# Kernel optimization log

Hardware: AMD Instinct MI355X
Metric: run time of the kernel (lower is better)

The kernel has to match this reference:

```python
import jax, jax.numpy as jnp
import numpy as np

ALPHA = 0.2      # LeakyReLU negative slope
BN_EPS = 1e-5    # torch BatchNorm1d default eps

N_NODES = 50000
N_EDGES = 1600000
DIM_IN = 128
DIM_HID = 64
DIM_OUT = 128
NUM_HEADS = 8


def gat_layer(feat, src, dst, W, a, gamma, beta):
    """One GATLayer forward (dropout disabled, BatchNorm in training mode
    i.e. normalized with batch statistics over the node dimension)."""
    n = feat.shape[0]
    dh = W.shape[1]
    msg = feat @ W                                  # [N, dh]
    attn_src = msg @ a[:dh]                         # [N]
    attn_dst = msg @ a[dh:]                         # [N]
    scores = jax.nn.leaky_relu(attn_src[src] + attn_dst[dst], ALPHA)  # [E]
    scores = scores - scores.max()                  # global max-subtract (as in source)
    e = jnp.exp(scores)                             # [E]
    denom = jax.ops.segment_sum(e, dst, num_segments=n) + 1e-10       # [N]
    coef = e / denom[dst]                           # [E] segment-softmax
    out = jax.ops.segment_sum(msg[src] * coef[:, None], dst, num_segments=n)  # [N, dh]
    # BatchNorm1d (training-mode batch stats, biased variance)
    mean = out.mean(axis=0)
    var = out.var(axis=0)
    out = (out - mean) * jax.lax.rsqrt(var + BN_EPS) * gamma + beta
    return out


def setup_inputs() -> dict:
    key = jax.random.key(0)
    ks = jax.random.split(key, 10)
    feat = jax.random.normal(ks[0], (N_NODES, DIM_IN), dtype=jnp.float32)
    edges = jax.random.randint(ks[1], (2, N_EDGES), 0, N_NODES)

    def xavier(k, shape):
        fan_in, fan_out = shape[0], shape[-1]
        lim = np.sqrt(6.0 / (fan_in + fan_out)).astype(np.float32)
        return jax.random.uniform(k, shape, jnp.float32, -lim, lim)

    W_heads = xavier(ks[2], (NUM_HEADS, DIM_IN, DIM_HID))
    a_heads = xavier(ks[3], (NUM_HEADS, 2 * DIM_HID))
    gamma_h = jnp.ones((NUM_HEADS, DIM_HID), jnp.float32)
    beta_h = jnp.zeros((NUM_HEADS, DIM_HID), jnp.float32)
    W_out = xavier(ks[4], (NUM_HEADS * DIM_HID, DIM_OUT))
    a_out = xavier(ks[5], (2 * DIM_OUT,))
    gamma_o = jnp.ones((DIM_OUT,), jnp.float32)
    beta_o = jnp.zeros((DIM_OUT,), jnp.float32)
    W_res = xavier(ks[6], (DIM_IN, DIM_OUT))
    b_res = jnp.zeros((DIM_OUT,), jnp.float32)
    return {"feat": feat, "edges": edges, "W_heads": W_heads, "a_heads": a_heads,
            "gamma_h": gamma_h, "beta_h": beta_h, "W_out": W_out, "a_out": a_out,
            "gamma_o": gamma_o, "beta_o": beta_o, "W_res": W_res, "b_res": b_res}


def reference(feat, edges, W_heads, a_heads, gamma_h, beta_h,
              W_out, a_out, gamma_o, beta_o, W_res, b_res):
    src, dst = edges[0], edges[1]
    # python loop over a small fixed number of heads keeps peak memory low
    head_outs = [gat_layer(feat, src, dst, W_heads[h], a_heads[h], gamma_h[h], beta_h[h])
                 for h in range(NUM_HEADS)]
    x = jnp.concatenate(head_outs, axis=-1)          # [N, H*dh]
    x = gat_layer(x, src, dst, W_out, a_out, gamma_o, beta_o)  # [N, dout]
    x = x + feat @ W_res + b_res                     # residual Linear
    return x
```

## Files before the change

### kernel.cpp

```cpp
#include <hip/hip_runtime.h>
#include <math.h>

#define N_NODES 50000
#define N_EDGES 1600000
#define DIM_IN  128
#define DIM_HID 64
#define NHEADS  8
#define HDIM    (NHEADS*DIM_HID)
#define DIM_OUT 128
#define SMBLK   1024
#define MAXBLK  512
#define LDK     72
#define INV_N   2e-5f
#define CSBLK   400

typedef __attribute__((ext_vector_type(2))) unsigned short us2;
typedef __attribute__((ext_vector_type(4))) unsigned short us4;
typedef __attribute__((ext_vector_type(8))) unsigned short us8;
typedef __attribute__((ext_vector_type(8))) short bf16x8;
typedef __attribute__((ext_vector_type(4))) float f32x4;

__device__ __forceinline__ float leaky(float x) { return x >= 0.f ? x : 0.2f * x; }
__device__ __forceinline__ float bf2f(unsigned short h) {
  return __uint_as_float(((unsigned)h) << 16);
}
__device__ __forceinline__ unsigned short f2bf(float f) {
  unsigned u = __float_as_uint(f);
  unsigned r = (u + 0x7fffu + ((u >> 16) & 1u)) >> 16;
  return (unsigned short)r;
}
__device__ __forceinline__ float bn_scale(float sum, float sq, float g) {
  float mean = sum * INV_N;
  float var = sq * INV_N - mean * mean;
  return g * rsqrtf(var + 1e-5f);
}

__global__ void prep_kernel(const float* __restrict__ feat, const float* __restrict__ Wh,
                            const float* __restrict__ Wres,
                            unsigned short* __restrict__ feat_bf,
                            unsigned short* __restrict__ Bt1,
                            unsigned short* __restrict__ Btr) {
  int b = blockIdx.x;
  if (b < 6250) {
    int i = b * 256 + threadIdx.x;
    float4 v = *reinterpret_cast<const float4*>(&feat[(size_t)i * 4]);
    us4 o;
    o[0] = f2bf(v.x); o[1] = f2bf(v.y); o[2] = f2bf(v.z); o[3] = f2bf(v.w);
    *reinterpret_cast<us4*>(&feat_bf[(size_t)i * 4]) = o;
  } else if (b < 6506) {
    int idx = (b - 6250) * 256 + threadIdx.x;
    int n = idx >> 7, k = idx & 127;
    Bt1[idx] = f2bf(Wh[(n >> 6) * (DIM_IN * DIM_HID) + k * DIM_HID + (n & 63)]);
  } else {
    int idx = (b - 6506) * 256 + threadIdx.x;
    int n = idx >> 7, k = idx & 127;
    Btr[idx] = f2bf(Wres[k * DIM_OUT + n]);
  }
}

__global__ void foldw2_kernel(const float* __restrict__ W,
                              const float* __restrict__ colsum, const float* __restrict__ colsq,
                              const float* __restrict__ gamma,
                              unsigned short* __restrict__ Bt) {
  int idx = blockIdx.x * 256 + threadIdx.x;
  if (idx >= DIM_OUT * HDIM) return;
  int n = idx >> 9, k = idx & 511;
  float sc = bn_scale(colsum[k], colsq[k], gamma[k]);
  Bt[idx] = f2bf(W[k * DIM_OUT + n] * sc);
}

__global__ void bias2_kernel(const float* __restrict__ W,
                             const float* __restrict__ colsum, const float* __restrict__ colsq,
                             const float* __restrict__ gamma, const float* __restrict__ beta,
                             float* __restrict__ bias2) {
  int j = threadIdx.x;
  if (j >= DIM_OUT) return;
  float s = 0.f;
  for (int c = 0; c < HDIM; ++c) {
    float mean = colsum[c] * INV_N;
    float sc = bn_scale(colsum[c], colsq[c], gamma[c]);
    float shift = beta[c] - mean * sc;
    s = fmaf(shift, W[c * DIM_OUT + j], s);
  }
  bias2[j] = s;
}

template<int OUTBF>
__global__ __launch_bounds__(256) void gemm_mfma(
    const unsigned short* __restrict__ A, const unsigned short* __restrict__ Bt,
    void* __restrict__ Cout, const float* __restrict__ bias,
    int M, int N, int K) {
  __shared__ unsigned short As[128 * LDK];
  __shared__ unsigned short Bs[128 * LDK];
  const int tid = threadIdx.x;
  const int lane = tid & 63, wid = tid >> 6;
  const int wr = wid >> 1, wc = wid & 1;
  const int l15 = lane & 15, lhi = lane >> 4;
  const int m0 = blockIdx.y * 128, n0 = blockIdx.x * 128;
  const int srow = tid >> 3;
  const int sc8 = (tid - srow) & 7;
  f32x4 acc[4][4];
#pragma unroll
  for (int i = 0; i < 4; ++i)
#pragma unroll
    for (int j = 0; j < 4; ++j) acc[i][j] = f32x4{0.f, 0.f, 0.f, 0.f};

  for (int k0 = 0; k0 < K; k0 += 64) {
    __syncthreads();
#pragma unroll
    for (int p = 0; p < 4; ++p) {
      int row = p * 32 + srow;
      us8 va = {0, 0, 0, 0, 0, 0, 0, 0};
      int gr = m0 + row;
      if (gr < M) va = *reinterpret_cast<const us8*>(&A[(size_t)gr * K + k0 + sc8 * 8]);
      *reinterpret_cast<us8*>(&As[row * LDK + sc8 * 8]) = va;
      us8 vb = {0, 0, 0, 0, 0, 0, 0, 0};
      int gn = n0 + row;
      if (gn < N) vb = *reinterpret_cast<const us8*>(&Bt[(size_t)gn * K + k0 + sc8 * 8]);
      *reinterpret_cast<us8*>(&Bs[row * LDK + sc8 * 8]) = vb;
    }
    __syncthreads();
#pragma unroll
    for (int kk = 0; kk < 2; ++kk) {
      bf16x8 af[4], bfr[4];
#pragma unroll
      for (int i = 0; i < 4; ++i)
        af[i] = *reinterpret_cast<const bf16x8*>(&As[(wr * 64 + i * 16 + l15) * LDK + kk * 32 + lhi * 8]);
#pragma unroll
      for (int j = 0; j < 4; ++j)
        bfr[j] = *reinterpret_cast<const bf16x8*>(&Bs[(wc * 64 + j * 16 + l15) * LDK + kk * 32 + lhi * 8]);
#pragma unroll
      for (int i = 0; i < 4; ++i)
#pragma unroll
        for (int j = 0; j < 4; ++j)
          acc[i][j] = __builtin_amdgcn_mfma_f32_16x16x32_bf16(af[i], bfr[j], acc[i][j], 0, 0, 0);
    }
  }
#pragma unroll
  for (int j = 0; j < 4; ++j) {
    int col = n0 + wc * 64 + j * 16 + l15;
    float bb = bias ? bias[col] : 0.f;
#pragma unroll
    for (int i = 0; i < 4; ++i) {
      f32x4 v = acc[i][j];
#pragma unroll
      for (int t = 0; t < 4; ++t) {
        int row = m0 + wr * 64 + i * 16 + lhi * 4 + t;
        if (row < M) {
          float o = v[t] + bb;
          if (OUTBF) ((unsigned short*)Cout)[(size_t)row * N + col] = f2bf(o);
          else       ((float*)Cout)[(size_t)row * N + col] = o;
        }
      }
    }
  }
}

__global__ __launch_bounds__(256) void attn1_kernel(
    const unsigned short* __restrict__ msg, const float* __restrict__ a_heads,
    float* __restrict__ asrc, float* __restrict__ adst, int Nn) {
  int lane = threadIdx.x & 63;
  int n = blockIdx.x * 4 + (threadIdx.x >> 6);
  if (n >= Nn) return;
  us8 v = *reinterpret_cast<const us8*>(&msg[(size_t)n * HDIM + lane * 8]);
  int h = lane >> 3, p0 = (lane & 7) * 8;
  float s = 0.f, d = 0.f;
#pragma unroll
  for (int j = 0; j < 8; ++j) {
    float f = bf2f(v[j]);
    s = fmaf(f, a_heads[h * 128 + p0 + j], s);
    d = fmaf(f, a_heads[h * 128 + 64 + p0 + j], d);
  }
  s += __shfl_xor(s, 1, 64); s += __shfl_xor(s, 2, 64); s += __shfl_xor(s, 4, 64);
  d += __shfl_xor(d, 1, 64); d += __shfl_xor(d, 2, 64); d += __shfl_xor(d, 4, 64);
  if ((lane & 7) == 0) { asrc[n * 8 + h] = s; adst[n * 8 + h] = d; }
}

__global__ __launch_bounds__(256) void attn2_kernel(
    const unsigned short* __restrict__ msg, const float* __restrict__ a_out,
    float* __restrict__ asrc, float* __restrict__ adst, int Nn) {
  int lane = threadIdx.x & 63;
  int n = blockIdx.x * 4 + (threadIdx.x >> 6);
  if (n >= Nn) return;
  us2 v = *reinterpret_cast<const us2*>(&msg[(size_t)n * 128 + lane * 2]);
  float f0 = bf2f(v[0]), f1 = bf2f(v[1]);
  float s = f0 * a_out[2 * lane] + f1 * a_out[2 * lane + 1];
  float d = f0 * a_out[128 + 2 * lane] + f1 * a_out[128 + 2 * lane + 1];
#pragma unroll
  for (int off = 32; off; off >>= 1) {
    s += __shfl_xor(s, off, 64);
    d += __shfl_xor(d, off, 64);
  }
  if (lane == 0) { asrc[n] = s; adst[n] = d; }
}

__global__ void hist_kernel(const int* __restrict__ edst, int* __restrict__ counts, int E) {
  for (int e = blockIdx.x * blockDim.x + threadIdx.x; e < E; e += gridDim.x * blockDim.x)
    atomicAdd(&counts[edst[e]], 1);
}

__global__ __launch_bounds__(256) void scan1_kernel(
    const int* __restrict__ counts, int* __restrict__ rowptr, int* __restrict__ bsum, int n) {
  __shared__ int wsum[4];
  int b0 = blockIdx.x * 1024;
  int t = threadIdx.x;
  int lane = t & 63, w = t >> 6;
  int v[4]; int s = 0;
#pragma unroll
  for (int i = 0; i < 4; ++i) {
    int idx = b0 + t * 4 + i;
    v[i] = (idx < n) ? counts[idx] : 0;
    s += v[i];
  }
  int x = s;
#pragma unroll
  for (int off = 1; off < 64; off <<= 1) {
    int y = __shfl_up(x, off, 64);
    if (lane >= off) x += y;
  }
  if (lane == 63) wsum[w] = x;
  __syncthreads();
  int wof = 0;
  for (int i = 0; i < w; ++i) wof += wsum[i];
  int run = wof + x - s;
#pragma unroll
  for (int i = 0; i < 4; ++i) {
    int idx = b0 + t * 4 + i;
    if (idx < n) rowptr[idx] = run;
    run += v[i];
  }
  if (t == 255) bsum[blockIdx.x] = wof + x;
}

__global__ void scan2_kernel(int* __restrict__ bsum, int nb) {
  int t = threadIdx.x;
  int v = (t < nb) ? bsum[t] : 0;
  int x = v;
#pragma unroll
  for (int off = 1; off < 64; off <<= 1) {
    int y = __shfl_up(x, off, 64);
    if (t >= off) x += y;
  }
  if (t < nb) bsum[t] = x - v;
}

__global__ void scan3_kernel(int* __restrict__ rowptr, const int* __restrict__ bsum, int n) {
  int i = blockIdx.x * 256 + threadIdx.x;
  if (i < n) rowptr[i] += bsum[i >> 10];
  else if (i == n) rowptr[n] = N_EDGES;
}

__global__ __launch_bounds__(256) void scatter_max1_kernel(
    const int* __restrict__ esrc, const int* __restrict__ edst,
    const float* __restrict__ asrc, const float* __restrict__ adst,
    const int* __restrict__ rowptr, int* __restrict__ cursor,
    int* __restrict__ colsrc, float* __restrict__ part, int E) {
  float m[8];
#pragma unroll
  for (int h = 0; h < 8; ++h) m[h] = -3.4e38f;
  for (int e = blockIdx.x * blockDim.x + threadIdx.x; e < E; e += gridDim.x * blockDim.x) {
    int s = esrc[e], d = edst[e];
    int pos = rowptr[d] + atomicAdd(&cursor[d], 1);
    colsrc[pos] = s;
    float4 s0 = *reinterpret_cast<const float4*>(&asrc[(size_t)s * 8]);
    float4 s1 = *reinterpret_cast<const float4*>(&asrc[(size_t)s * 8 + 4]);
    float4 d0 = *reinterpret_cast<const float4*>(&adst[(size_t)d * 8]);
    float4 d1 = *reinterpret_cast<const float4*>(&adst[(size_t)d * 8 + 4]);
    float xs[8] = {s0.x + d0.x, s0.y + d0.y, s0.z + d0.z, s0.w + d0.w,
                   s1.x + d1.x, s1.y + d1.y, s1.z + d1.z, s1.w + d1.w};
#pragma unroll
    for (int h = 0; h < 8; ++h) m[h] = fmaxf(m[h], leaky(xs[h]));
  }
#pragma unroll
  for (int h = 0; h < 8; ++h)
#pragma unroll
    for (int off = 32; off; off >>= 1) m[h] = fmaxf(m[h], __shfl_xor(m[h], off, 64));
  __shared__ float sm[4][8];
  int wv = threadIdx.x >> 6, ln = threadIdx.x & 63;
  if (ln == 0)
#pragma unroll
    for (int h = 0; h < 8; ++h) sm[wv][h] = m[h];
  __syncthreads();
  if (threadIdx.x < 8) {
    int h = threadIdx.x;
    part[blockIdx.x * 8 + h] =
        fmaxf(fmaxf(sm[0][h], sm[1][h]), fmaxf(sm[2][h], sm[3][h]));
  }
}

__global__ void max1_final_kernel(const float* __restrict__ part, float* __restrict__ maxv, int nblk) {
  int t = threadIdx.x;
  int h = t & 7, k = t >> 3;
  float m = -3.4e38f;
  for (int i = k; i < nblk; i += 8) m = fmaxf(m, part[i * 8 + h]);
  m = fmaxf(m, __shfl_xor(m, 8, 64));
  m = fmaxf(m, __shfl_xor(m, 16, 64));
  m = fmaxf(m, __shfl_xor(m, 32, 64));
  if (t < 8) maxv[t] = m;
}

__global__ __launch_bounds__(256) void max2_part_kernel(
    const int* __restrict__ esrc, const int* __restrict__ edst,
    const float* __restrict__ asrc, const float* __restrict__ adst,
    float* __restrict__ part, int E) {
  float m = -3.4e38f;
  for (int e = blockIdx.x * blockDim.x + threadIdx.x; e < E; e += gridDim.x * blockDim.x) {
    float x = asrc[esrc[e]] + adst[edst[e]];
    m = fmaxf(m, leaky(x));
  }
#pragma unroll
  for (int off = 32; off; off >>= 1) m = fmaxf(m, __shfl_xor(m, off, 64));
  __shared__ float sm[4];
  int wv = threadIdx.x >> 6, ln = threadIdx.x & 63;
  if (ln == 0) sm[wv] = m;
  __syncthreads();
  if (threadIdx.x == 0)
    part[blockIdx.x] = fmaxf(fmaxf(sm[0], sm[1]), fmaxf(sm[2], sm[3]));
}

__global__ void max2_final_kernel(const float* __restrict__ part, float* __restrict__ maxv, int nblk) {
  int t = threadIdx.x;
  float m = -3.4e38f;
  for (int i = t; i < nblk; i += 64) m = fmaxf(m, part[i]);
#pragma unroll
  for (int off = 32; off; off >>= 1) m = fmaxf(m, __shfl_xor(m, off, 64));
  if (t == 0) maxv[0] = m;
}

__global__ __launch_bounds__(128) void agg1_kernel(
    const unsigned short* __restrict__ msg, const float* __restrict__ asrc,
    const float* __restrict__ adst, const float* __restrict__ maxv,
    const int* __restrict__ rowptr, const int* __restrict__ colsrc,
    unsigned short* __restrict__ out) {
  int n = blockIdx.x;
  int tid = threadIdx.x;
  __shared__ int s_sh[64];
  __shared__ float coef_sh[64][8];
  __shared__ float hdr[16];
  if (tid < 8) {
    hdr[tid] = maxv[tid];
    hdr[8 + tid] = adst[(size_t)n * 8 + tid];
  }
  __syncthreads();
  const int h = tid >> 4;
  const int e0 = rowptr[n], e1 = rowptr[n + 1];
  float4 acc = make_float4(0.f, 0.f, 0.f, 0.f);
  float dsum = 0.f;
  for (int base = e0; base < e1; base += 64) {
    int cnt = min(64, e1 - base);
    __syncthreads();
#pragma unroll
    for (int q = 0; q < 4; ++q) {
      int slot = q * 128 + tid;
      int el = slot >> 3, hh = slot & 7;
      if (el < cnt) {
        int s = colsrc[base + el];
        if (hh == 0) s_sh[el] = s;
        float x = asrc[(size_t)s * 8 + hh] + hdr[8 + hh];
        x = x >= 0.f ? x : 0.2f * x;
        coef_sh[el][hh] = __expf(x - hdr[hh]);
      }
    }
    __syncthreads();
    int e = 0;
    for (; e + 4 <= cnt; e += 4) {
      int sA = s_sh[e], sB = s_sh[e + 1], sC = s_sh[e + 2], sD = s_sh[e + 3];
      us4 ma = *reinterpret_cast<const us4*>(&msg[(size_t)sA * HDIM + tid * 4]);
      us4 mb = *reinterpret_cast<const us4*>(&msg[(size_t)sB * HDIM + tid * 4]);
      us4 mc = *reinterpret_cast<const us4*>(&msg[(size_t)sC * HDIM + tid * 4]);
      us4 md = *reinterpret_cast<const us4*>(&msg[(size_t)sD * HDIM + tid * 4]);
      float ca = coef_sh[e][h], cb = coef_sh[e + 1][h];
      float cc = coef_sh[e + 2][h], cd = coef_sh[e + 3][h];
      dsum += (ca + cb) + (cc + cd);
      acc.x = fmaf(bf2f(ma[0]), ca, acc.x); acc.y = fmaf(bf2f(ma[1]), ca, acc.y);
      acc.z = fmaf(bf2f(ma[2]), ca, acc.z); acc.w = fmaf(bf2f(ma[3]), ca, acc.w);
      acc.x = fmaf(bf2f(mb[0]), cb, acc.x); acc.y = fmaf(bf2f(mb[1]), cb, acc.y);
      acc.z = fmaf(bf2f(mb[2]), cb, acc.z); acc.w = fmaf(bf2f(mb[3]), cb, acc.w);
      acc.x = fmaf(bf2f(mc[0]), cc, acc.x); acc.y = fmaf(bf2f(mc[1]), cc, acc.y);
      acc.z = fmaf(bf2f(mc[2]), cc, acc.z); acc.w = fmaf(bf2f(mc[3]), cc, acc.w);
      acc.x = fmaf(bf2f(md[0]), cd, acc.x); acc.y = fmaf(bf2f(md[1]), cd, acc.y);
      acc.z = fmaf(bf2f(md[2]), cd, acc.z); acc.w = fmaf(bf2f(md[3]), cd, acc.w);
    }
    for (; e < cnt; ++e) {
      int s = s_sh[e];
      float c = coef_sh[e][h];
      dsum += c;
      us4 m4 = *reinterpret_cast<const us4*>(&msg[(size_t)s * HDIM + tid * 4]);
      acc.x = fmaf(bf2f(m4[0]), c, acc.x); acc.y = fmaf(bf2f(m4[1]), c, acc.y);
      acc.z = fmaf(bf2f(m4[2]), c, acc.z); acc.w = fmaf(bf2f(m4[3]), c, acc.w);
    }
  }
  float inv = 1.0f / (dsum + 1e-10f);
  us4 o;
  o[0] = f2bf(acc.x * inv); o[1] = f2bf(acc.y * inv);
  o[2] = f2bf(acc.z * inv); o[3] = f2bf(acc.w * inv);
  *reinterpret_cast<us4*>(&out[(size_t)n * HDIM + tid * 4]) = o;
}

__global__ __launch_bounds__(256) void agg2_kernel(
    const unsigned short* __restrict__ msg, const float* __restrict__ asrc,
    const float* __restrict__ adst, const float* __restrict__ maxv,
    const int* __restrict__ rowptr, const int* __restrict__ colsrc,
    float* __restrict__ out) {
  int wv = threadIdx.x >> 6, ln = threadIdx.x & 63;
  int n = blockIdx.x * 4 + wv;
  float M = maxv[0];
  float ad = adst[n];
  int e0 = rowptr[n], e1 = rowptr[n + 1];
  float a0 = 0.f, a1 = 0.f, ds = 0.f;
  for (int base = e0; base < e1; base += 64) {
    int cnt = min(64, e1 - base);
    int s_reg = 0; float c_reg = 0.f;
    if (ln < cnt) {
      s_reg = colsrc[base + ln];
      float x = asrc[s_reg] + ad;
      x = x >= 0.f ? x : 0.2f * x;
      c_reg = __expf(x - M);
    }
    int e = 0;
    for (; e + 4 <= cnt; e += 4) {
      int s0 = __shfl(s_reg, e, 64),     s1 = __shfl(s_reg, e + 1, 64);
      int s2 = __shfl(s_reg, e + 2, 64), s3 = __shfl(s_reg, e + 3, 64);
      float c0 = __shfl(c_reg, e, 64),     c1 = __shfl(c_reg, e + 1, 64);
      float c2 = __shfl(c_reg, e + 2, 64), c3 = __shfl(c_reg, e + 3, 64);
      us2 m0 = *reinterpret_cast<const us2*>(&msg[(size_t)s0 * 128 + 2 * ln]);
      us2 m1 = *reinterpret_cast<const us2*>(&msg[(size_t)s1 * 128 + 2 * ln]);
      us2 m2 = *reinterpret_cast<const us2*>(&msg[(size_t)s2 * 128 + 2 * ln]);
      us2 m3 = *reinterpret_cast<const us2*>(&msg[(size_t)s3 * 128 + 2 * ln]);
      ds += (c0 + c1) + (c2 + c3);
      a0 = fmaf(bf2f(m0[0]), c0, a0); a1 = fmaf(bf2f(m0[1]), c0, a1);
      a0 = fmaf(bf2f(m1[0]), c1, a0); a1 = fmaf(bf2f(m1[1]), c1, a1);
      a0 = fmaf(bf2f(m2[0]), c2, a0); a1 = fmaf(bf2f(m2[1]), c2, a1);
      a0 = fmaf(bf2f(m3[0]), c3, a0); a1 = fmaf(bf2f(m3[1]), c3, a1);
    }
    for (; e < cnt; ++e) {
      int s = __shfl(s_reg, e, 64);
      float c = __shfl(c_reg, e, 64);
      us2 m = *reinterpret_cast<const us2*>(&msg[(size_t)s * 128 + 2 * ln]);
      ds += c;
      a0 = fmaf(bf2f(m[0]), c, a0);
      a1 = fmaf(bf2f(m[1]), c, a1);
    }
  }
  float inv = 1.0f / (ds + 1e-10f);
  float2 r; r.x = a0 * inv; r.y = a1 * inv;
  *reinterpret_cast<float2*>(&out[(size_t)n * 128 + 2 * ln]) = r;
}

__global__ __launch_bounds__(256) void colstats_bf512_kernel(
    const unsigned short* __restrict__ X, float* __restrict__ sums,
    float* __restrict__ sqs, int M) {
  int tid = threadIdx.x;
  int cg = tid & 63;
  int wv = tid >> 6;
  int rows = (M + gridDim.x - 1) / gridDim.x;
  int r0 = blockIdx.x * rows;
  int r1 = min(M, r0 + rows);
  float s[8], q[8];
#pragma unroll
  for (int j = 0; j < 8; ++j) { s[j] = 0.f; q[j] = 0.f; }
  for (int r = r0 + wv; r < r1; r += 4) {
    us8 v = *reinterpret_cast<const us8*>(&X[(size_t)r * 512 + cg * 8]);
#pragma unroll
    for (int j = 0; j < 8; ++j) {
      float f = bf2f(v[j]);
      s[j] += f; q[j] = fmaf(f, f, q[j]);
    }
  }
  __shared__ float shs[3][512];
  __shared__ float shq[3][512];
  if (wv > 0) {
#pragma unroll
    for (int j = 0; j < 8; ++j) {
      shs[wv - 1][cg * 8 + j] = s[j];
      shq[wv - 1][cg * 8 + j] = q[j];
    }
  }
  __syncthreads();
  if (wv == 0) {
#pragma unroll
    for (int j = 0; j < 8; ++j) {
      int c = cg * 8 + j;
      atomicAdd(&sums[c], s[j] + shs[0][c] + shs[1][c] + shs[2][c]);
      atomicAdd(&sqs[c],  q[j] + shq[0][c] + shq[1][c] + shq[2][c]);
    }
  }
}

__global__ __launch_bounds__(256) void colstats_f128_kernel(
    const float* __restrict__ X, float* __restrict__ sums,
    float* __restrict__ sqs, int M) {
  int tid = threadIdx.x;
  int g = tid & 31;
  int slot = tid >> 5;
  int rows = (M + gridDim.x - 1) / gridDim.x;
  int r0 = blockIdx.x * rows;
  int r1 = min(M, r0 + rows);
  float s[4] = {0.f, 0.f, 0.f, 0.f}, q[4] = {0.f, 0.f, 0.f, 0.f};
  for (int r = r0 + slot; r < r1; r += 8) {
    float4 v = *reinterpret_cast<const float4*>(&X[(size_t)r * 128 + g * 4]);
    s[0] += v.x; q[0] = fmaf(v.x, v.x, q[0]);
    s[1] += v.y; q[1] = fmaf(v.y, v.y, q[1]);
    s[2] += v.z; q[2] = fmaf(v.z, v.z, q[2]);
    s[3] += v.w; q[3] = fmaf(v.w, v.w, q[3]);
  }
#pragma unroll
  for (int j = 0; j < 4; ++j) {
    s[j] += __shfl_xor(s[j], 32, 64);
    q[j] += __shfl_xor(q[j], 32, 64);
  }
  __shared__ float shs[3][128];
  __shared__ float shq[3][128];
  int wv = tid >> 6, ln = tid & 63;
  if (wv > 0 && ln < 32) {
#pragma unroll
    for (int j = 0; j < 4; ++j) {
      shs[wv - 1][g * 4 + j] = s[j];
      shq[wv - 1][g * 4 + j] = q[j];
    }
  }
  __syncthreads();
  if (wv == 0 && ln < 32) {
#pragma unroll
    for (int j = 0; j < 4; ++j) {
      int c = g * 4 + j;
      atomicAdd(&sums[c], s[j] + shs[0][c] + shs[1][c] + shs[2][c]);
      atomicAdd(&sqs[c],  q[j] + shq[0][c] + shq[1][c] + shq[2][c]);
    }
  }
}

__global__ void final_kernel(float* __restrict__ out, const float* __restrict__ resid,
                             const float* __restrict__ colsum, const float* __restrict__ colsq,
                             const float* __restrict__ gamma, const float* __restrict__ beta,
                             int total) {
  for (int i = blockIdx.x * blockDim.x + threadIdx.x; i < total; i += gridDim.x * blockDim.x) {
    int c = i & 127;
    float mean = colsum[c] * INV_N;
    float sc = bn_scale(colsum[c], colsq[c], gamma[c]);
    float sh = beta[c] - mean * sc;
    out[i] = fmaf(out[i], sc, sh) + resid[i];
  }
}

extern "C" void kernel_launch(void* const* d_in, const int* in_sizes, int n_in,
                              void* d_out, int out_size, void* d_ws, size_t ws_size,
                              hipStream_t stream) {
  const float* feat    = (const float*)d_in[0];
  const int*   edges   = (const int*)d_in[1];
  const int*   esrc    = edges;
  const int*   edst    = edges + N_EDGES;
  const float* W_heads = (const float*)d_in[2];
  const float* a_heads = (const float*)d_in[3];
  const float* gamma_h = (const float*)d_in[4];
  const float* beta_h  = (const float*)d_in[5];
  const float* W_out   = (const float*)d_in[6];
  const float* a_out   = (const float*)d_in[7];
  const float* gamma_o = (const float*)d_in[8];
  const float* beta_o  = (const float*)d_in[9];
  const float* W_res   = (const float*)d_in[10];
  const float* b_res   = (const float*)d_in[11];
  float* out = (float*)d_out;

  char* ws = (char*)d_ws;
  size_t off = 0;
  auto alloc = [&](size_t bytes) {
    void* p = ws + off;
    off = (off + bytes + 255) & ~(size_t)255;
    return p;
  };
  unsigned short* msg1    = (unsigned short*)alloc((size_t)N_NODES * HDIM * 2);
  unsigned short* out1_bf = (unsigned short*)alloc((size_t)N_NODES * HDIM * 2);
  unsigned short* feat_bf = (unsigned short*)alloc((size_t)N_NODES * DIM_IN * 2);
  float*    resid  = (float*)alloc((size_t)N_NODES * DIM_OUT * 4);
  float*    asrc1  = (float*)alloc((size_t)N_NODES * NHEADS * 4);
  float*    adst1  = (float*)alloc((size_t)N_NODES * NHEADS * 4);
  int*      counts = (int*)alloc((size_t)N_NODES * 4);
  int*      cursor = (int*)alloc((size_t)N_NODES * 4);
  int*      rowptr = (int*)alloc((size_t)(N_NODES + 1) * 4);
  int*      colsrc = (int*)alloc((size_t)N_EDGES * 4);
  int*      bsum   = (int*)alloc(64 * 4);
  float*    part   = (float*)alloc((size_t)SMBLK * 8 * 4);
  float*    maxv1  = (float*)alloc(8 * 4);
  float*    maxv2  = (float*)alloc(4);
  float*    colsum = (float*)alloc(HDIM * 4);
  float*    colsq  = (float*)alloc(HDIM * 4);
  unsigned short* Bt1 = (unsigned short*)alloc((size_t)HDIM * DIM_IN * 2);
  unsigned short* Bt2 = (unsigned short*)alloc((size_t)DIM_OUT * HDIM * 2);
  unsigned short* Btr = (unsigned short*)alloc((size_t)DIM_OUT * DIM_IN * 2);
  float*    bias2  = (float*)alloc(DIM_OUT * 4);
  unsigned short* msg2 = msg1;
  float* asrc2 = asrc1; float* adst2 = adst1;
  (void)n_in; (void)in_sizes; (void)out_size; (void)ws_size;

  hipMemsetAsync(counts, 0, (char*)rowptr - (char*)counts, stream);
  hipMemsetAsync(colsum, 0, 4096, stream);

  prep_kernel<<<6570, 256, 0, stream>>>(feat, W_heads, W_res, feat_bf, Bt1, Btr);

  dim3 g1(HDIM / 128, (N_NODES + 127) / 128);
  gemm_mfma<1><<<g1, 256, 0, stream>>>(feat_bf, Bt1, msg1, nullptr, N_NODES, HDIM, DIM_IN);
  attn1_kernel<<<(N_NODES + 3) / 4, 256, 0, stream>>>(msg1, a_heads, asrc1, adst1, N_NODES);

  hist_kernel<<<2048, 256, 0, stream>>>(edst, counts, N_EDGES);
  int nsb = (N_NODES + 1023) / 1024;
  scan1_kernel<<<nsb, 256, 0, stream>>>(counts, rowptr, bsum, N_NODES);
  scan2_kernel<<<1, 64, 0, stream>>>(bsum, nsb);
  scan3_kernel<<<(N_NODES + 256) / 256, 256, 0, stream>>>(rowptr, bsum, N_NODES);

  scatter_max1_kernel<<<SMBLK, 256, 0, stream>>>(esrc, edst, asrc1, adst1, rowptr,
                                                 cursor, colsrc, part, N_EDGES);
  max1_final_kernel<<<1, 64, 0, stream>>>(part, maxv1, SMBLK);
  agg1_kernel<<<N_NODES, 128, 0, stream>>>(msg1, asrc1, adst1, maxv1, rowptr, colsrc, out1_bf);

  colstats_bf512_kernel<<<CSBLK, 256, 0, stream>>>(out1_bf, colsum, colsq, N_NODES);
  foldw2_kernel<<<(DIM_OUT * HDIM + 255) / 256, 256, 0, stream>>>(W_out, colsum, colsq, gamma_h, Bt2);
  bias2_kernel<<<1, 128, 0, stream>>>(W_out, colsum, colsq, gamma_h, beta_h, bias2);

  dim3 g2(DIM_OUT / 128, (N_NODES + 127) / 128);
  gemm_mfma<1><<<g2, 256, 0, stream>>>(out1_bf, Bt2, msg2, bias2, N_NODES, DIM_OUT, HDIM);
  attn2_kernel<<<(N_NODES + 3) / 4, 256, 0, stream>>>(msg2, a_out, asrc2, adst2, N_NODES);

  max2_part_kernel<<<MAXBLK, 256, 0, stream>>>(esrc, edst, asrc2, adst2, part, N_EDGES);
  max2_final_kernel<<<1, 64, 0, stream>>>(part, maxv2, MAXBLK);
  agg2_kernel<<<N_NODES / 4, 256, 0, stream>>>(msg2, asrc2, adst2, maxv2, rowptr, colsrc, out);

  gemm_mfma<0><<<g2, 256, 0, stream>>>(feat_bf, Btr, resid, b_res, N_NODES, DIM_OUT, DIM_IN);

  hipMemsetAsync(colsum, 0, 4096, stream);
  colstats_f128_kernel<<<CSBLK, 256, 0, stream>>>(out, colsum, colsq, N_NODES);
  final_kernel<<<2048, 256, 0, stream>>>(out, resid, colsum, colsq, gamma_o, beta_o,
                                         N_NODES * DIM_OUT);
}
```

Baseline: 796.3 us.

## Fuse histogram, scans and residual GEMM; rewrite agg1 as wave-per-node

The edge histogram moves into the prep kernel as extra blocks, and the two scan fix-up kernels are merged into one. The residual GEMM is co-launched with the second-layer GEMM through a z-dimension split. agg1 changes from one 128-thread block per node with shared-memory staging to one wavefront per node, using shuffles for the coefficients and 16-byte loads. The aim is fewer launches, no barriers in the aggregation and more memory-level parallelism, at the cost of a runtime outbf branch in the GEMM and less latency hiding per node in agg1.

```diff
diff --git a/kernel.cpp b/kernel.cpp
--- a/kernel.cpp
+++ b/kernel.cpp
@@ -10,6 +10,7 @@
 #define DIM_OUT 128
 #define SMBLK   1024
 #define MAXBLK  512
+#define HISTBLK 2048
 #define LDK     72
 #define INV_N   2e-5f
 #define CSBLK   400
@@ -36,10 +37,11 @@
 }
 
 __global__ void prep_kernel(const float* __restrict__ feat, const float* __restrict__ Wh,
-                            const float* __restrict__ Wres,
+                            const float* __restrict__ Wres, const int* __restrict__ edst,
                             unsigned short* __restrict__ feat_bf,
                             unsigned short* __restrict__ Bt1,
-                            unsigned short* __restrict__ Btr) {
+                            unsigned short* __restrict__ Btr,
+                            int* __restrict__ counts) {
   int b = blockIdx.x;
   if (b < 6250) {
     int i = b * 256 + threadIdx.x;
@@ -51,10 +53,14 @@
     int idx = (b - 6250) * 256 + threadIdx.x;
     int n = idx >> 7, k = idx & 127;
     Bt1[idx] = f2bf(Wh[(n >> 6) * (DIM_IN * DIM_HID) + k * DIM_HID + (n & 63)]);
-  } else {
+  } else if (b < 6570) {
     int idx = (b - 6506) * 256 + threadIdx.x;
     int n = idx >> 7, k = idx & 127;
     Btr[idx] = f2bf(Wres[k * DIM_OUT + n]);
+  } else {
+    int bid = b - 6570;
+    for (int e = bid * 256 + threadIdx.x; e < N_EDGES; e += HISTBLK * 256)
+      atomicAdd(&counts[edst[e]], 1);
   }
 }
 
@@ -85,11 +91,10 @@
   bias2[j] = s;
 }
 
-template<int OUTBF>
-__global__ __launch_bounds__(256) void gemm_mfma(
+__device__ __forceinline__ void gemm_body(
     const unsigned short* __restrict__ A, const unsigned short* __restrict__ Bt,
     void* __restrict__ Cout, const float* __restrict__ bias,
-    int M, int N, int K) {
+    int M, int N, int K, int outbf) {
   __shared__ unsigned short As[128 * LDK];
   __shared__ unsigned short Bs[128 * LDK];
   const int tid = threadIdx.x;
@@ -148,12 +153,28 @@
         int row = m0 + wr * 64 + i * 16 + lhi * 4 + t;
         if (row < M) {
           float o = v[t] + bb;
-          if (OUTBF) ((unsigned short*)Cout)[(size_t)row * N + col] = f2bf(o);
+          if (outbf) ((unsigned short*)Cout)[(size_t)row * N + col] = f2bf(o);
           else       ((float*)Cout)[(size_t)row * N + col] = o;
         }
       }
     }
   }
+}
+
+__global__ __launch_bounds__(256) void gemm_single(
+    const unsigned short* __restrict__ A, const unsigned short* __restrict__ Bt,
+    void* __restrict__ Cout, const float* __restrict__ bias,
+    int M, int N, int K, int outbf) {
+  gemm_body(A, Bt, Cout, bias, M, N, K, outbf);
+}
+
+__global__ __launch_bounds__(256) void gemm_dual(
+    const unsigned short* __restrict__ A0, const unsigned short* __restrict__ Bt0,
+    void* __restrict__ C0, const float* __restrict__ b0, int K0,
+    const unsigned short* __restrict__ A1, const unsigned short* __restrict__ Bt1,
+    void* __restrict__ C1, const float* __restrict__ b1, int K1) {
+  if (blockIdx.z == 0) gemm_body(A0, Bt0, C0, b0, N_NODES, DIM_OUT, K0, 1);
+  else                 gemm_body(A1, Bt1, C1, b1, N_NODES, DIM_OUT, K1, 0);
 }
 
 __global__ __launch_bounds__(256) void attn1_kernel(
@@ -194,11 +215,6 @@
   if (lane == 0) { asrc[n] = s; adst[n] = d; }
 }
 
-__global__ void hist_kernel(const int* __restrict__ edst, int* __restrict__ counts, int E) {
-  for (int e = blockIdx.x * blockDim.x + threadIdx.x; e < E; e += gridDim.x * blockDim.x)
-    atomicAdd(&counts[edst[e]], 1);
-}
-
 __global__ __launch_bounds__(256) void scan1_kernel(
     const int* __restrict__ counts, int* __restrict__ rowptr, int* __restrict__ bsum, int n) {
   __shared__ int wsum[4];
@@ -232,22 +248,25 @@
   if (t == 255) bsum[blockIdx.x] = wof + x;
 }
 
-__global__ void scan2_kernel(int* __restrict__ bsum, int nb) {
-  int t = threadIdx.x;
-  int v = (t < nb) ? bsum[t] : 0;
-  int x = v;
-#pragma unroll
-  for (int off = 1; off < 64; off <<= 1) {
-    int y = __shfl_up(x, off, 64);
-    if (t >= off) x += y;
-  }
-  if (t < nb) bsum[t] = x - v;
-}
-
-__global__ void scan3_kernel(int* __restrict__ rowptr, const int* __restrict__ bsum, int n) {
-  int i = blockIdx.x * 256 + threadIdx.x;
-  if (i < n) rowptr[i] += bsum[i >> 10];
-  else if (i == n) rowptr[n] = N_EDGES;
+__global__ __launch_bounds__(256) void scan23_kernel(
+    int* __restrict__ rowptr, const int* __restrict__ bsum, int n) {
+  __shared__ int carry_sh;
+  int b = blockIdx.x, t = threadIdx.x;
+  if (t < 64) {
+    int v = (t < b) ? bsum[t] : 0;
+#pragma unroll
+    for (int off = 32; off; off >>= 1) v += __shfl_xor(v, off, 64);
+    if (t == 0) carry_sh = v;
+  }
+  __syncthreads();
+  int carry = carry_sh;
+  int i0 = b * 1024;
+#pragma unroll
+  for (int q = 0; q < 4; ++q) {
+    int i = i0 + q * 256 + t;
+    if (i < n) rowptr[i] += carry;
+  }
+  if (b == gridDim.x - 1 && t == 0) rowptr[n] = N_EDGES;
 }
 
 __global__ __launch_bounds__(256) void scatter_max1_kernel(
@@ -327,74 +346,62 @@
   if (t == 0) maxv[0] = m;
 }
 
-__global__ __launch_bounds__(128) void agg1_kernel(
+__global__ __launch_bounds__(256) void agg1_kernel(
     const unsigned short* __restrict__ msg, const float* __restrict__ asrc,
     const float* __restrict__ adst, const float* __restrict__ maxv,
     const int* __restrict__ rowptr, const int* __restrict__ colsrc,
     unsigned short* __restrict__ out) {
-  int n = blockIdx.x;
-  int tid = threadIdx.x;
-  __shared__ int s_sh[64];
-  __shared__ float coef_sh[64][8];
-  __shared__ float hdr[16];
-  if (tid < 8) {
-    hdr[tid] = maxv[tid];
-    hdr[8 + tid] = adst[(size_t)n * 8 + tid];
-  }
-  __syncthreads();
-  const int h = tid >> 4;
-  const int e0 = rowptr[n], e1 = rowptr[n + 1];
-  float4 acc = make_float4(0.f, 0.f, 0.f, 0.f);
-  float dsum = 0.f;
-  for (int base = e0; base < e1; base += 64) {
-    int cnt = min(64, e1 - base);
-    __syncthreads();
-#pragma unroll
-    for (int q = 0; q < 4; ++q) {
-      int slot = q * 128 + tid;
-      int el = slot >> 3, hh = slot & 7;
-      if (el < cnt) {
-        int s = colsrc[base + el];
-        if (hh == 0) s_sh[el] = s;
-        float x = asrc[(size_t)s * 8 + hh] + hdr[8 + hh];
-        x = x >= 0.f ? x : 0.2f * x;
-        coef_sh[el][hh] = __expf(x - hdr[hh]);
-      }
-    }
-    __syncthreads();
-    int e = 0;
-    for (; e + 4 <= cnt; e += 4) {
-      int sA = s_sh[e], sB = s_sh[e + 1], sC = s_sh[e + 2], sD = s_sh[e + 3];
-      us4 ma = *reinterpret_cast<const us4*>(&msg[(size_t)sA * HDIM + tid * 4]);
-      us4 mb = *reinterpret_cast<const us4*>(&msg[(size_t)sB * HDIM + tid * 4]);
-      us4 mc = *reinterpret_cast<const us4*>(&msg[(size_t)sC * HDIM + tid * 4]);
-      us4 md = *reinterpret_cast<const us4*>(&msg[(size_t)sD * HDIM + tid * 4]);
-      float ca = coef_sh[e][h], cb = coef_sh[e + 1][h];
-      float cc = coef_sh[e + 2][h], cd = coef_sh[e + 3][h];
-      dsum += (ca + cb) + (cc + cd);
-      acc.x = fmaf(bf2f(ma[0]), ca, acc.x); acc.y = fmaf(bf2f(ma[1]), ca, acc.y);
-      acc.z = fmaf(bf2f(ma[2]), ca, acc.z); acc.w = fmaf(bf2f(ma[3]), ca, acc.w);
-      acc.x = fmaf(bf2f(mb[0]), cb, acc.x); acc.y = fmaf(bf2f(mb[1]), cb, acc.y);
-      acc.z = fmaf(bf2f(mb[2]), cb, acc.z); acc.w = fmaf(bf2f(mb[3]), cb, acc.w);
-      acc.x = fmaf(bf2f(mc[0]), cc, acc.x); acc.y = fmaf(bf2f(mc[1]), cc, acc.y);
-      acc.z = fmaf(bf2f(mc[2]), cc, acc.z); acc.w = fmaf(bf2f(mc[3]), cc, acc.w);
-      acc.x = fmaf(bf2f(md[0]), cd, acc.x); acc.y = fmaf(bf2f(md[1]), cd, acc.y);
-      acc.z = fmaf(bf2f(md[2]), cd, acc.z); acc.w = fmaf(bf2f(md[3]), cd, acc.w);
-    }
-    for (; e < cnt; ++e) {
-      int s = s_sh[e];
-      float c = coef_sh[e][h];
-      dsum += c;
-      us4 m4 = *reinterpret_cast<const us4*>(&msg[(size_t)s * HDIM + tid * 4]);
-      acc.x = fmaf(bf2f(m4[0]), c, acc.x); acc.y = fmaf(bf2f(m4[1]), c, acc.y);
-      acc.z = fmaf(bf2f(m4[2]), c, acc.z); acc.w = fmaf(bf2f(m4[3]), c, acc.w);
-    }
-  }
-  float inv = 1.0f / (dsum + 1e-10f);
-  us4 o;
-  o[0] = f2bf(acc.x * inv); o[1] = f2bf(acc.y * inv);
-  o[2] = f2bf(acc.z * inv); o[3] = f2bf(acc.w * inv);
-  *reinterpret_cast<us4*>(&out[(size_t)n * HDIM + tid * 4]) = o;
+  int wv = threadIdx.x >> 6, l = threadIdx.x & 63;
+  int n = blockIdx.x * 4 + wv;
+  const int h = l >> 3;
+  const int eloc = l & 7;
+  const int hbase = l & 56;
+  float M = maxv[h];
+  float ad = adst[(size_t)n * 8 + h];
+  int e0 = rowptr[n], e1 = rowptr[n + 1];
+  float acc[8];
+#pragma unroll
+  for (int j = 0; j < 8; ++j) acc[j] = 0.f;
+  float ds = 0.f;
+  int base = e0;
+  for (; base + 8 <= e1; base += 8) {
+    int sreg = colsrc[base + eloc];
+    float x = asrc[(size_t)sreg * 8 + h] + ad;
+    x = x >= 0.f ? x : 0.2f * x;
+    float creg = __expf(x - M);
+#pragma unroll
+    for (int e = 0; e < 8; ++e) {
+      float c = __shfl(creg, hbase | e, 64);
+      int s = __shfl(sreg, e, 64);
+      ds += c;
+      us8 m = *reinterpret_cast<const us8*>(&msg[(size_t)s * HDIM + l * 8]);
+#pragma unroll
+      for (int j = 0; j < 8; ++j) acc[j] = fmaf(bf2f(m[j]), c, acc[j]);
+    }
+  }
+  if (base < e1) {
+    int cnt = e1 - base;
+    int sreg = 0; float creg = 0.f;
+    if (eloc < cnt) {
+      sreg = colsrc[base + eloc];
+      float x = asrc[(size_t)sreg * 8 + h] + ad;
+      x = x >= 0.f ? x : 0.2f * x;
+      creg = __expf(x - M);
+    }
+    for (int e = 0; e < cnt; ++e) {
+      float c = __shfl(creg, hbase | e, 64);
+      int s = __shfl(sreg, e, 64);
+      ds += c;
+      us8 m = *reinterpret_cast<const us8*>(&msg[(size_t)s * HDIM + l * 8]);
+#pragma unroll
+      for (int j = 0; j < 8; ++j) acc[j] = fmaf(bf2f(m[j]), c, acc[j]);
+    }
+  }
+  float inv = 1.0f / (ds + 1e-10f);
+  us8 o;
+#pragma unroll
+  for (int j = 0; j < 8; ++j) o[j] = f2bf(acc[j] * inv);
+  *reinterpret_cast<us8*>(&out[(size_t)n * HDIM + l * 8]) = o;
 }
 
 __global__ __launch_bounds__(256) void agg2_kernel(
@@ -596,36 +603,34 @@
   hipMemsetAsync(counts, 0, (char*)rowptr - (char*)counts, stream);
   hipMemsetAsync(colsum, 0, 4096, stream);
 
-  prep_kernel<<<6570, 256, 0, stream>>>(feat, W_heads, W_res, feat_bf, Bt1, Btr);
+  prep_kernel<<<6570 + HISTBLK, 256, 0, stream>>>(feat, W_heads, W_res, edst,
+                                                  feat_bf, Bt1, Btr, counts);
 
   dim3 g1(HDIM / 128, (N_NODES + 127) / 128);
-  gemm_mfma<1><<<g1, 256, 0, stream>>>(feat_bf, Bt1, msg1, nullptr, N_NODES, HDIM, DIM_IN);
+  gemm_single<<<g1, 256, 0, stream>>>(feat_bf, Bt1, msg1, nullptr, N_NODES, HDIM, DIM_IN, 1);
   attn1_kernel<<<(N_NODES + 3) / 4, 256, 0, stream>>>(msg1, a_heads, asrc1, adst1, N_NODES);
 
-  hist_kernel<<<2048, 256, 0, stream>>>(edst, counts, N_EDGES);
   int nsb = (N_NODES + 1023) / 1024;
   scan1_kernel<<<nsb, 256, 0, stream>>>(counts, rowptr, bsum, N_NODES);
-  scan2_kernel<<<1, 64, 0, stream>>>(bsum, nsb);
-  scan3_kernel<<<(N_NODES + 256) / 256, 256, 0, stream>>>(rowptr, bsum, N_NODES);
+  scan23_kernel<<<nsb, 256, 0, stream>>>(rowptr, bsum, N_NODES);
 
   scatter_max1_kernel<<<SMBLK, 256, 0, stream>>>(esrc, edst, asrc1, adst1, rowptr,
                                                  cursor, colsrc, part, N_EDGES);
   max1_final_kernel<<<1, 64, 0, stream>>>(part, maxv1, SMBLK);
-  agg1_kernel<<<N_NODES, 128, 0, stream>>>(msg1, asrc1, adst1, maxv1, rowptr, colsrc, out1_bf);
+  agg1_kernel<<<N_NODES / 4, 256, 0, stream>>>(msg1, asrc1, adst1, maxv1, rowptr, colsrc, out1_bf);
 
   colstats_bf512_kernel<<<CSBLK, 256, 0, stream>>>(out1_bf, colsum, colsq, N_NODES);
   foldw2_kernel<<<(DIM_OUT * HDIM + 255) / 256, 256, 0, stream>>>(W_out, colsum, colsq, gamma_h, Bt2);
   bias2_kernel<<<1, 128, 0, stream>>>(W_out, colsum, colsq, gamma_h, beta_h, bias2);
 
-  dim3 g2(DIM_OUT / 128, (N_NODES + 127) / 128);
-  gemm_mfma<1><<<g2, 256, 0, stream>>>(out1_bf, Bt2, msg2, bias2, N_NODES, DIM_OUT, HDIM);
+  dim3 g2d(1, (N_NODES + 127) / 128, 2);
+  gemm_dual<<<g2d, 256, 0, stream>>>(out1_bf, Bt2, msg2, bias2, HDIM,
+                                     feat_bf, Btr, resid, b_res, DIM_IN);
   attn2_kernel<<<(N_NODES + 3) / 4, 256, 0, stream>>>(msg2, a_out, asrc2, adst2, N_NODES);
 
   max2_part_kernel<<<MAXBLK, 256, 0, stream>>>(esrc, edst, asrc2, adst2, part, N_EDGES);
   max2_final_kernel<<<1, 64, 0, stream>>>(part, maxv2, MAXBLK);
   agg2_kernel<<<N_NODES / 4, 256, 0, stream>>>(msg2, asrc2, adst2, maxv2, rowptr, colsrc, out);
-
-  gemm_mfma<0><<<g2, 256, 0, stream>>>(feat_bf, Btr, resid, b_res, N_NODES, DIM_OUT, DIM_IN);
 
   hipMemsetAsync(colsum, 0, 4096, stream);
   colstats_f128_kernel<<<CSBLK, 256, 0, stream>>>(out, colsum, colsq, N_NODES);
```

Result: no change. 780.9 us (-1.9%).
